# Kernel tuning notes

Measured on AMD Instinct MI355X. Metric: run time of the kernel, lower is better.

The kernel has to match this reference:

```python
import jax, jax.numpy as jnp
import numpy as np

B, M, N, E = 64, 100, 6400, 102400   # graphs, nodes/graph, total nodes, edges
H, D, EMB, IMG, NC = 4, 512, 768, 1024, 2
HD = H * D
EPS = 1e-5


def _bn2(x, g, b, m, v):
    # BatchNorm1d eval mode on [B, C]
    return (x - m) / jnp.sqrt(v + EPS) * g + b


def _bn3(x, g, b, m, v):
    # BatchNorm1d eval mode on [B, C, L] -> channel dim is axis 1 (node index)
    return (x - m[None, :, None]) / jnp.sqrt(v + EPS)[None, :, None] * g[None, :, None] + b[None, :, None]


def _gat(feat, src, dst, W, al, ar, bias):
    # DGL GATConv (eval: feat_drop is identity). feat: [N, F_in]
    h = (feat @ W.T).reshape(-1, H, D)                 # [N, H, D]
    el = (h * al[None]).sum(-1)                         # [N, H]
    er = (h * ar[None]).sum(-1)                         # [N, H]
    e = jax.nn.leaky_relu(el[src] + er[dst], negative_slope=0.2)  # [E, H]
    mx = jax.ops.segment_max(e, dst, num_segments=N)
    a = jnp.exp(e - mx[dst])
    s = jax.ops.segment_sum(a, dst, num_segments=N)
    alpha = a / s[dst]                                  # edge softmax over incoming edges
    out = jax.ops.segment_sum(h[src] * alpha[:, :, None], dst, num_segments=N)  # [N, H, D]
    return out + bias.reshape(1, H, D)


def setup_inputs() -> dict:
    key = jax.random.key(0)
    ks = iter(jax.random.split(key, 80))
    n = lambda *s: jax.random.normal(next(ks), s, dtype=jnp.float32)

    def bn(c):
        return (1.0 + 0.1 * n(c), 0.1 * n(c), 0.1 * n(c),
                0.5 + jax.random.uniform(next(ks), (c,), dtype=jnp.float32))

    s = 0.02
    inp = {}
    inp['img_embedding'] = n(B, IMG)
    inp['func_text_embedding'] = n(B, EMB)
    inp['unix_emb'] = n(N, EMB)
    inp['pos_emb'] = jax.random.uniform(next(ks), (N, 4), dtype=jnp.float32)
    inp['src'] = jax.random.randint(next(ks), (E,), 0, N)
    inp['dst'] = jax.random.randint(next(ks), (E,), 0, N)
    inp['gat1_W'] = n(HD, EMB) * s; inp['gat1_al'] = n(H, D) * 0.1; inp['gat1_ar'] = n(H, D) * 0.1; inp['gat1_b'] = jnp.zeros(HD)
    inp['gat2_W'] = n(HD, HD) * s; inp['gat2_al'] = n(H, D) * 0.1; inp['gat2_ar'] = n(H, D) * 0.1; inp['gat2_b'] = jnp.zeros(HD)
    inp['fc_W'] = n(D, HD) * s; inp['fc_b'] = jnp.zeros(D)
    inp['hidden_W'] = n(8, D, D) * s; inp['hidden_b'] = jnp.zeros((8, D))
    inp['bn_text_g'], inp['bn_text_b'], inp['bn_text_m'], inp['bn_text_v'] = bn(EMB)
    inp['fc_text_W'] = n(D, EMB) * s; inp['fc_text_b'] = jnp.zeros(D)
    inp['swin_g'], inp['swin_b'], inp['swin_m'], inp['swin_v'] = bn(IMG)
    inp['swinfc_W'] = n(D, IMG) * s; inp['swinfc_b'] = jnp.zeros(D)
    inp['bngat_g'], inp['bngat_b'], inp['bngat_m'], inp['bngat_v'] = bn(M)
    inp['fc_gat_W'] = n(480, D) * s; inp['fc_gat_b'] = jnp.zeros(480)
    inp['bnbb_g'], inp['bnbb_b'], inp['bnbb_m'], inp['bnbb_v'] = bn(M)
    inp['fc_bbox_W'] = n(32, 4) * s; inp['fc_bbox_b'] = jnp.zeros(32)
    inp['fbn_g'], inp['fbn_b'], inp['fbn_m'], inp['fbn_v'] = bn(3 * D)
    inp['final_W'] = n(NC, 3 * D) * s; inp['final_b'] = jnp.zeros(NC)
    return inp


def reference(img_embedding, func_text_embedding, unix_emb, pos_emb, src, dst,
              gat1_W, gat1_al, gat1_ar, gat1_b, gat2_W, gat2_al, gat2_ar, gat2_b,
              fc_W, fc_b, hidden_W, hidden_b,
              bn_text_g, bn_text_b, bn_text_m, bn_text_v, fc_text_W, fc_text_b,
              swin_g, swin_b, swin_m, swin_v, swinfc_W, swinfc_b,
              bngat_g, bngat_b, bngat_m, bngat_v, fc_gat_W, fc_gat_b,
              bnbb_g, bnbb_b, bnbb_m, bnbb_v, fc_bbox_W, fc_bbox_b,
              fbn_g, fbn_b, fbn_m, fbn_v, final_W, final_b):
    # image branch
    x = jax.nn.elu(_bn2(img_embedding, swin_g, swin_b, swin_m, swin_v) @ swinfc_W.T + swinfc_b)
    # text branch
    ft = jax.nn.elu(_bn2(func_text_embedding, bn_text_g, bn_text_b, bn_text_m, bn_text_v) @ fc_text_W.T + fc_text_b)
    # graph branch: two stacked GATConv layers (dropout is identity in eval)
    h = _gat(unix_emb, src, dst, gat1_W, gat1_al, gat1_ar, gat1_b).reshape(N, HD)
    h = _gat(h, src, dst, gat2_W, gat2_al, gat2_ar, gat2_b).reshape(N, HD)
    h = jax.nn.elu(h @ fc_W.T + fc_b)
    for i in range(8):
        h = jax.nn.elu(h @ hidden_W[i].T + hidden_b[i])
    # unbatch + pad to max_node=100 -> pure reshape (all graphs have exactly M nodes)
    h_i = h.reshape(B, M, D)
    pos_i = pos_emb.reshape(B, M, 4)
    h_i = jax.nn.elu(_bn3(h_i, bngat_g, bngat_b, bngat_m, bngat_v) @ fc_gat_W.T + fc_gat_b)      # [B, M, 480]
    pos_i = jax.nn.elu(_bn3(pos_i, bnbb_g, bnbb_b, bnbb_m, bnbb_v) @ fc_bbox_W.T + fc_bbox_b)    # [B, M, 32]
    h_feature = jnp.concatenate([h_i, pos_i], axis=2).mean(axis=1)                                # [B, 512]
    all_feats = jnp.concatenate([x, h_feature, ft], axis=1)                                       # [B, 1536]
    return _bn2(all_feats, fbn_g, fbn_b, fbn_m, fbn_v) @ final_W.T + final_b
```

## Files before the change

kernel.cpp:

```cpp
#include <hip/hip_runtime.h>
#include <math.h>

#define Bg   64
#define Mg   100
#define Ng   6400
#define Eg   102400
#define Hh   4
#define Dd   512
#define HDd  2048
#define EMBd 768
#define IMGd 1024
#define EPSc 1e-5f

typedef __bf16 bf16x8 __attribute__((ext_vector_type(8)));
typedef float  f32x4  __attribute__((ext_vector_type(4)));

__device__ __forceinline__ float eluf(float x) { return x > 0.f ? x : expm1f(x); }

__device__ __forceinline__ unsigned short f2bf(float x) {
    unsigned int u = __builtin_bit_cast(unsigned int, x);
    u += 0x7FFFu + ((u >> 16) & 1u);
    return (unsigned short)(u >> 16);
}
__device__ __forceinline__ float bf2f(unsigned short s) {
    return __builtin_bit_cast(float, ((unsigned int)s) << 16);
}

__device__ __forceinline__ void gld16(const void* g, void* l) {
    __builtin_amdgcn_global_load_lds(
        (const __attribute__((address_space(1))) void*)g,
        (__attribute__((address_space(3))) void*)l, 16, 0, 0);
}

__global__ __launch_bounds__(256)
void gemm_bf16(const unsigned short* __restrict__ A,
               const unsigned short* __restrict__ W,
               const float* __restrict__ bias, void* __restrict__ C,
               int M, int N, int K, int act, int outbf)
{
    __shared__ __align__(16) unsigned short As[128 * 32];
    __shared__ __align__(16) unsigned short Bs[128 * 32];
    const int tid  = threadIdx.x;
    const int lane = tid & 63, wid = tid >> 6;
    const int bm = blockIdx.y * 128, bn = blockIdx.x * 128;
    const int wm = (wid >> 1) * 64, wn = (wid & 1) * 64;
    const int lrow = lane >> 2;
    const int lcol = (lane & 3) << 3;

    f32x4 acc[4][4] = {};

    const int ra = wid * 32;
    const unsigned short* gA0 = A + (size_t)(bm + ra + lrow) * K + lcol;
    const unsigned short* gA1 = A + (size_t)(bm + ra + 16 + lrow) * K + lcol;
    int rb0 = bn + ra + lrow;       if (rb0 >= N) rb0 = N - 1;
    int rb1 = bn + ra + 16 + lrow;  if (rb1 >= N) rb1 = N - 1;
    const unsigned short* gB0 = W + (size_t)rb0 * K + lcol;
    const unsigned short* gB1 = W + (size_t)rb1 * K + lcol;
    unsigned short* lA0 = &As[(ra)      * 32];
    unsigned short* lA1 = &As[(ra + 16) * 32];
    unsigned short* lB0 = &Bs[(ra)      * 32];
    unsigned short* lB1 = &Bs[(ra + 16) * 32];

    const int frow = lane & 15;
    const int quad = (lane >> 4) << 3;

    for (int k0 = 0; k0 < K; k0 += 32) {
        gld16(gA0 + k0, lA0);
        gld16(gA1 + k0, lA1);
        gld16(gB0 + k0, lB0);
        gld16(gB1 + k0, lB1);
        __syncthreads();
        bf16x8 af[4], bfr[4];
#pragma unroll
        for (int i = 0; i < 4; ++i)
            af[i]  = *(const bf16x8*)&As[(wm + i * 16 + frow) * 32 + quad];
#pragma unroll
        for (int i = 0; i < 4; ++i)
            bfr[i] = *(const bf16x8*)&Bs[(wn + i * 16 + frow) * 32 + quad];
#pragma unroll
        for (int mi = 0; mi < 4; ++mi)
#pragma unroll
            for (int ni = 0; ni < 4; ++ni)
                acc[mi][ni] = __builtin_amdgcn_mfma_f32_16x16x32_bf16(
                    af[mi], bfr[ni], acc[mi][ni], 0, 0, 0);
        __syncthreads();
    }

    const int crow0 = bm + wm + ((lane >> 4) << 2);
    const int ccol0 = bn + wn + (lane & 15);
#pragma unroll
    for (int mi = 0; mi < 4; ++mi) {
#pragma unroll
        for (int ni = 0; ni < 4; ++ni) {
            int col = ccol0 + ni * 16;
            if (col >= N) continue;
            float bv = bias ? bias[col] : 0.f;
#pragma unroll
            for (int r = 0; r < 4; ++r) {
                int row = crow0 + mi * 16 + r;
                float v = acc[mi][ni][r] + bv;
                if (act) v = eluf(v);
                if (outbf) ((unsigned short*)C)[(size_t)row * N + col] = f2bf(v);
                else       ((float*)C)[(size_t)row * N + col] = v;
            }
        }
    }
}

__global__ __launch_bounds__(256)
void gemm_bf16_t64(const unsigned short* __restrict__ A,
                   const unsigned short* __restrict__ W,
                   const float* __restrict__ bias, void* __restrict__ C,
                   int M, int N, int K, int act, int outbf)
{
    __shared__ __align__(16) unsigned short As[64 * 32];
    __shared__ __align__(16) unsigned short Bs[64 * 32];
    const int tid  = threadIdx.x;
    const int lane = tid & 63, wid = tid >> 6;
    const int bm = blockIdx.y * 64, bn = blockIdx.x * 64;
    const int wm = (wid >> 1) * 32, wn = (wid & 1) * 32;
    const int lrow = lane >> 2;
    const int lcol = (lane & 3) << 3;

    f32x4 acc[2][2] = {};

    const int ra = wid * 16;
    const unsigned short* gA = A + (size_t)(bm + ra + lrow) * K + lcol;
    int rb = bn + ra + lrow; if (rb >= N) rb = N - 1;
    const unsigned short* gB = W + (size_t)rb * K + lcol;
    unsigned short* lA = &As[ra * 32];
    unsigned short* lB = &Bs[ra * 32];

    const int frow = lane & 15;
    const int quad = (lane >> 4) << 3;

    for (int k0 = 0; k0 < K; k0 += 32) {
        gld16(gA + k0, lA);
        gld16(gB + k0, lB);
        __syncthreads();
        bf16x8 af0 = *(const bf16x8*)&As[(wm + frow) * 32 + quad];
        bf16x8 af1 = *(const bf16x8*)&As[(wm + 16 + frow) * 32 + quad];
        bf16x8 bf0 = *(const bf16x8*)&Bs[(wn + frow) * 32 + quad];
        bf16x8 bf1 = *(const bf16x8*)&Bs[(wn + 16 + frow) * 32 + quad];
        acc[0][0] = __builtin_amdgcn_mfma_f32_16x16x32_bf16(af0, bf0, acc[0][0], 0, 0, 0);
        acc[0][1] = __builtin_amdgcn_mfma_f32_16x16x32_bf16(af0, bf1, acc[0][1], 0, 0, 0);
        acc[1][0] = __builtin_amdgcn_mfma_f32_16x16x32_bf16(af1, bf0, acc[1][0], 0, 0, 0);
        acc[1][1] = __builtin_amdgcn_mfma_f32_16x16x32_bf16(af1, bf1, acc[1][1], 0, 0, 0);
        __syncthreads();
    }

    const int crow0 = bm + wm + ((lane >> 4) << 2);
    const int ccol0 = bn + wn + (lane & 15);
#pragma unroll
    for (int mi = 0; mi < 2; ++mi) {
#pragma unroll
        for (int ni = 0; ni < 2; ++ni) {
            int col = ccol0 + ni * 16;
            if (col >= N) continue;
            float bv = bias ? bias[col] : 0.f;
#pragma unroll
            for (int r = 0; r < 4; ++r) {
                int row = crow0 + mi * 16 + r;
                float v = acc[mi][ni][r] + bv;
                if (act) v = eluf(v);
                if (outbf) ((unsigned short*)C)[(size_t)row * N + col] = f2bf(v);
                else       ((float*)C)[(size_t)row * N + col] = v;
            }
        }
    }
}

__global__ __launch_bounds__(256)
void gemm_t64_fcgat(const unsigned short* __restrict__ A,
                    const unsigned short* __restrict__ W,
                    const float* __restrict__ bfg, const float* __restrict__ wsum,
                    const float* __restrict__ bng, const float* __restrict__ bnb,
                    const float* __restrict__ bnm, const float* __restrict__ bnv,
                    float* __restrict__ Eout, int M, int N, int K)
{
    __shared__ __align__(16) unsigned short As[64 * 32];
    __shared__ __align__(16) unsigned short Bs[64 * 32];
    const int tid  = threadIdx.x;
    const int lane = tid & 63, wid = tid >> 6;
    const int bm = blockIdx.y * 64, bn = blockIdx.x * 64;
    const int wm = (wid >> 1) * 32, wn = (wid & 1) * 32;
    const int lrow = lane >> 2;
    const int lcol = (lane & 3) << 3;

    f32x4 acc[2][2] = {};

    const int ra = wid * 16;
    const unsigned short* gA = A + (size_t)(bm + ra + lrow) * K + lcol;
    int rb = bn + ra + lrow; if (rb >= N) rb = N - 1;
    const unsigned short* gB = W + (size_t)rb * K + lcol;
    unsigned short* lA = &As[ra * 32];
    unsigned short* lB = &Bs[ra * 32];

    const int frow = lane & 15;
    const int quad = (lane >> 4) << 3;

    for (int k0 = 0; k0 < K; k0 += 32) {
        gld16(gA + k0, lA);
        gld16(gB + k0, lB);
        __syncthreads();
        bf16x8 af0 = *(const bf16x8*)&As[(wm + frow) * 32 + quad];
        bf16x8 af1 = *(const bf16x8*)&As[(wm + 16 + frow) * 32 + quad];
        bf16x8 bf0 = *(const bf16x8*)&Bs[(wn + frow) * 32 + quad];
        bf16x8 bf1 = *(const bf16x8*)&Bs[(wn + 16 + frow) * 32 + quad];
        acc[0][0] = __builtin_amdgcn_mfma_f32_16x16x32_bf16(af0, bf0, acc[0][0], 0, 0, 0);
        acc[0][1] = __builtin_amdgcn_mfma_f32_16x16x32_bf16(af0, bf1, acc[0][1], 0, 0, 0);
        acc[1][0] = __builtin_amdgcn_mfma_f32_16x16x32_bf16(af1, bf0, acc[1][0], 0, 0, 0);
        acc[1][1] = __builtin_amdgcn_mfma_f32_16x16x32_bf16(af1, bf1, acc[1][1], 0, 0, 0);
        __syncthreads();
    }

    const int crow0 = bm + wm + ((lane >> 4) << 2);
    const int ccol0 = bn + wn + (lane & 15);
#pragma unroll
    for (int mi = 0; mi < 2; ++mi) {
#pragma unroll
        for (int r = 0; r < 4; ++r) {
            int row = crow0 + mi * 16 + r;
            int p = row % Mg;
            float sc = rsqrtf(bnv[p] + EPSc) * bng[p];
            float sh = bnb[p] - bnm[p] * sc;
#pragma unroll
            for (int ni = 0; ni < 2; ++ni) {
                int col = ccol0 + ni * 16;
                if (col < N) {
                    float v = sc * acc[mi][ni][r] + sh * wsum[col] + bfg[col];
                    Eout[(size_t)row * N + col] = eluf(v);
                }
            }
        }
    }
}

__global__ __launch_bounds__(256)
void wsum_kernel(const float* __restrict__ W, float* __restrict__ s)
{
    int row = (blockIdx.x << 2) + (threadIdx.x >> 6);
    int lane = threadIdx.x & 63;
    if (row >= 480) return;
    const float* p = W + (size_t)row * Dd;
    float a = 0.f;
    for (int k = lane; k < Dd; k += 64) a += p[k];
#pragma unroll
    for (int o = 32; o > 0; o >>= 1) a += __shfl_down(a, o, 64);
    if (lane == 0) s[row] = a;
}

__global__ __launch_bounds__(256)
void gemm_nt(const float* __restrict__ A, const float* __restrict__ W,
             const float* __restrict__ bias, float* __restrict__ C,
             int M, int N, int K, int act)
{
    __shared__ float As[16 * 68];
    __shared__ float Ws[16 * 68];
    const int tid = threadIdx.x;
    const int tx = tid & 15, ty = tid >> 4;
    const int bm = blockIdx.y * 64, bn = blockIdx.x * 64;
    const int lrow = tid >> 2;
    const int lk4  = (tid & 3) << 2;
    const int arow = bm + lrow;
    const int wrow = bn + lrow;
    const float* Aptr = A + (size_t)arow * K + lk4;
    const float* Wptr = W + (size_t)wrow * K + lk4;
    float acc[4][4] = {{0.f,0.f,0.f,0.f},{0.f,0.f,0.f,0.f},{0.f,0.f,0.f,0.f},{0.f,0.f,0.f,0.f}};

    for (int k0 = 0; k0 < K; k0 += 16) {
        float4 av = make_float4(0.f,0.f,0.f,0.f);
        float4 wv = make_float4(0.f,0.f,0.f,0.f);
        if (arow < M) av = *(const float4*)(Aptr + k0);
        if (wrow < N) wv = *(const float4*)(Wptr + k0);
        As[(lk4+0)*68 + lrow] = av.x;
        As[(lk4+1)*68 + lrow] = av.y;
        As[(lk4+2)*68 + lrow] = av.z;
        As[(lk4+3)*68 + lrow] = av.w;
        Ws[(lk4+0)*68 + lrow] = wv.x;
        Ws[(lk4+1)*68 + lrow] = wv.y;
        Ws[(lk4+2)*68 + lrow] = wv.z;
        Ws[(lk4+3)*68 + lrow] = wv.w;
        __syncthreads();
#pragma unroll
        for (int kk = 0; kk < 16; ++kk) {
            float4 a = *(const float4*)&As[kk*68 + (ty<<2)];
            float4 w = *(const float4*)&Ws[kk*68 + (tx<<2)];
            acc[0][0] += a.x*w.x; acc[0][1] += a.x*w.y; acc[0][2] += a.x*w.z; acc[0][3] += a.x*w.w;
            acc[1][0] += a.y*w.x; acc[1][1] += a.y*w.y; acc[1][2] += a.y*w.z; acc[1][3] += a.y*w.w;
            acc[2][0] += a.z*w.x; acc[2][1] += a.z*w.y; acc[2][2] += a.z*w.z; acc[2][3] += a.z*w.w;
            acc[3][0] += a.w*w.x; acc[3][1] += a.w*w.y; acc[3][2] += a.w*w.z; acc[3][3] += a.w*w.w;
        }
        __syncthreads();
    }

#pragma unroll
    for (int i = 0; i < 4; ++i) {
        int row = bm + (ty<<2) + i;
        int col = bn + (tx<<2);
        if (row < M && col < N) {
            float4 v;
            v.x = acc[i][0]; v.y = acc[i][1]; v.z = acc[i][2]; v.w = acc[i][3];
            if (bias) { v.x += bias[col]; v.y += bias[col+1]; v.z += bias[col+2]; v.w += bias[col+3]; }
            if (act == 1) { v.x = eluf(v.x); v.y = eluf(v.y); v.z = eluf(v.z); v.w = eluf(v.w); }
            *(float4*)(C + (size_t)row * N + col) = v;
        }
    }
}

struct CvtPack {
    const float* s[6];
    unsigned short* d[6];
    int n4[6];
};

__global__ void cvt_all(CvtPack p, int total4)
{
    int i = blockIdx.x * 256 + threadIdx.x;
    if (i >= total4) return;
#pragma unroll
    for (int k = 0; k < 6; ++k) {
        if (i < p.n4[k]) {
            float4 v = ((const float4*)p.s[k])[i];
            ushort4 o;
            o.x = f2bf(v.x); o.y = f2bf(v.y); o.z = f2bf(v.z); o.w = f2bf(v.w);
            ((ushort4*)p.d[k])[i] = o;
            return;
        }
        i -= p.n4[k];
    }
}

__global__ void bn_col(const float* __restrict__ x, const float* __restrict__ g,
                       const float* __restrict__ b, const float* __restrict__ m,
                       const float* __restrict__ v, float* __restrict__ y,
                       int rows, int cols)
{
    int i = blockIdx.x * 256 + threadIdx.x;
    if (i >= rows * cols) return;
    int c = i % cols;
    float inv = rsqrtf(v[c] + EPSc);
    y[i] = (x[i] - m[c]) * inv * g[c] + b[c];
}

__global__ void zero_i32(int* __restrict__ p, int n)
{
    int i = blockIdx.x * 256 + threadIdx.x;
    if (i < n) p[i] = 0;
}

__global__ void count_dst(const int* __restrict__ dst, int* __restrict__ counts, int E)
{
    int i = blockIdx.x * 256 + threadIdx.x;
    if (i < E) atomicAdd(&counts[dst[i]], 1);
}

__global__ __launch_bounds__(1024)
void scan_excl(const int* __restrict__ counts, int* __restrict__ offs,
               int* __restrict__ cursor, int n)
{
    const int T = 7;
    int tid = threadIdx.x;
    int base = tid * T;
    int v[T];
    int tot = 0;
#pragma unroll
    for (int j = 0; j < T; ++j) {
        int i = base + j;
        v[j] = (i < n) ? counts[i] : 0;
        tot += v[j];
    }
    int lane = tid & 63, w = tid >> 6;
    int incl = tot;
#pragma unroll
    for (int o = 1; o < 64; o <<= 1) {
        int t = __shfl_up(incl, o, 64);
        if (lane >= o) incl += t;
    }
    __shared__ int wtot[16];
    __shared__ int wbase[16];
    if (lane == 63) wtot[w] = incl;
    __syncthreads();
    if (tid == 0) {
        int s = 0;
        for (int i = 0; i < 16; ++i) { wbase[i] = s; s += wtot[i]; }
    }
    __syncthreads();
    int ex = wbase[w] + incl - tot;
#pragma unroll
    for (int j = 0; j < T; ++j) {
        int i = base + j;
        if (i < n) { offs[i] = ex; cursor[i] = ex; }
        ex += v[j];
    }
    if (tid == 1023) offs[n] = ex;
}

__global__ void scatter_edges(const int* __restrict__ dst, int* __restrict__ cursor,
                              int* __restrict__ eid, int E)
{
    int i = blockIdx.x * 256 + threadIdx.x;
    if (i < E) {
        int p = atomicAdd(&cursor[dst[i]], 1);
        eid[p] = i;
    }
}

__global__ __launch_bounds__(256)
void elr_kernel(const unsigned short* __restrict__ Hm, const float* __restrict__ al,
                const float* __restrict__ ar, float* __restrict__ el,
                float* __restrict__ er)
{
    int wid = threadIdx.x >> 6, lane = threadIdx.x & 63;
    int g = (blockIdx.x << 2) + wid;
    int n = g >> 2, h = g & 3;
    const unsigned short* hp = Hm + ((size_t)n << 11) + (h << 9) + (lane << 3);
    const float* alp = al + (h << 9) + (lane << 3);
    const float* arp = ar + (h << 9) + (lane << 3);
    ushort4 x0 = *(const ushort4*)hp;
    ushort4 x1 = *(const ushort4*)(hp + 4);
    float4 l0 = *(const float4*)alp, l1 = *(const float4*)(alp + 4);
    float4 r0 = *(const float4*)arp, r1 = *(const float4*)(arp + 4);
    float a0 = bf2f(x0.x), a1 = bf2f(x0.y), a2 = bf2f(x0.z), a3 = bf2f(x0.w);
    float a4 = bf2f(x1.x), a5 = bf2f(x1.y), a6 = bf2f(x1.z), a7 = bf2f(x1.w);
    float se = a0*l0.x + a1*l0.y + a2*l0.z + a3*l0.w + a4*l1.x + a5*l1.y + a6*l1.z + a7*l1.w;
    float sr = a0*r0.x + a1*r0.y + a2*r0.z + a3*r0.w + a4*r1.x + a5*r1.y + a6*r1.z + a7*r1.w;
#pragma unroll
    for (int o = 32; o > 0; o >>= 1) {
        se += __shfl_down(se, o, 64);
        sr += __shfl_down(sr, o, 64);
    }
    if (lane == 0) { el[g] = se; er[g] = sr; }
}

__global__ __launch_bounds__(256)
void gat_agg(const unsigned short* __restrict__ Hm, const float* __restrict__ el,
             const float* __restrict__ er, const int* __restrict__ src,
             const int* __restrict__ offs, const int* __restrict__ eid,
             const float* __restrict__ bias, unsigned short* __restrict__ out)
{
    int n = blockIdx.x;
    int tid = threadIdx.x;
    int beg = offs[n], end = offs[n + 1];
    int deg = end - beg;
    const int b0 = tid << 2;
    const int b1 = 1024 + (tid << 2);
    const int h0 = tid >> 7;
    const int h1 = h0 + 2;

    if (deg == 0) {
#pragma unroll
        for (int j = 0; j < 4; ++j) {
            out[((size_t)n << 11) + b0 + j] = f2bf(bias[b0 + j]);
            out[((size_t)n << 11) + b1 + j] = f2bf(bias[b1 + j]);
        }
        return;
    }

    __shared__ float m_sh[4], s_sh[4], al_sh[4];
    __shared__ int   src_sh[128];
    __shared__ float logit_sh[512];
    __shared__ float w_sh[512];

    if (tid < 4) { m_sh[tid] = -INFINITY; s_sh[tid] = 0.f; }
    float acc[8] = {0.f,0.f,0.f,0.f,0.f,0.f,0.f,0.f};
    __syncthreads();

    for (int c0 = 0; c0 < deg; c0 += 128) {
        int cnt = min(128, deg - c0);
        for (int i = tid; i < cnt; i += 256) src_sh[i] = src[eid[beg + c0 + i]];
        __syncthreads();
        for (int idx = tid; idx < (cnt << 2); idx += 256) {
            int i = idx >> 2, h = idx & 3;
            float x = el[(src_sh[i] << 2) + h] + er[(n << 2) + h];
            logit_sh[idx] = x > 0.f ? x : 0.2f * x;
        }
        __syncthreads();
        if (tid < 4) {
            float cm = -INFINITY;
            for (int i = 0; i < cnt; ++i) cm = fmaxf(cm, logit_sh[(i << 2) + tid]);
            float mn = fmaxf(m_sh[tid], cm);
            al_sh[tid] = expf(m_sh[tid] - mn);
            m_sh[tid] = mn;
        }
        __syncthreads();
        for (int idx = tid; idx < (cnt << 2); idx += 256)
            w_sh[idx] = expf(logit_sh[idx] - m_sh[idx & 3]);
        __syncthreads();
        if (tid < 4) {
            float cs = 0.f;
            for (int i = 0; i < cnt; ++i) cs += w_sh[(i << 2) + tid];
            s_sh[tid] = s_sh[tid] * al_sh[tid] + cs;
        }
        float r0 = al_sh[h0], r1 = al_sh[h1];
        acc[0] *= r0; acc[1] *= r0; acc[2] *= r0; acc[3] *= r0;
        acc[4] *= r1; acc[5] *= r1; acc[6] *= r1; acc[7] *= r1;
        for (int i = 0; i < cnt; ++i) {
            const unsigned short* hp = Hm + ((size_t)src_sh[i] << 11);
            ushort4 a = *(const ushort4*)(hp + b0);
            ushort4 b = *(const ushort4*)(hp + b1);
            float w0 = w_sh[(i << 2) + h0], w1 = w_sh[(i << 2) + h1];
            acc[0] += w0 * bf2f(a.x); acc[1] += w0 * bf2f(a.y);
            acc[2] += w0 * bf2f(a.z); acc[3] += w0 * bf2f(a.w);
            acc[4] += w1 * bf2f(b.x); acc[5] += w1 * bf2f(b.y);
            acc[6] += w1 * bf2f(b.z); acc[7] += w1 * bf2f(b.w);
        }
        __syncthreads();
    }

    float is0 = 1.f / s_sh[h0], is1 = 1.f / s_sh[h1];
#pragma unroll
    for (int j = 0; j < 4; ++j) {
        out[((size_t)n << 11) + b0 + j] = f2bf(acc[j] * is0 + bias[b0 + j]);
        out[((size_t)n << 11) + b1 + j] = f2bf(acc[4 + j] * is1 + bias[b1 + j]);
    }
}

__global__ __launch_bounds__(256)
void mean_kernel(const float* __restrict__ hg, const float* __restrict__ pos,
                 const float* __restrict__ bg, const float* __restrict__ bb_,
                 const float* __restrict__ bm_, const float* __restrict__ bv_,
                 const float* __restrict__ W, const float* __restrict__ bias,
                 float* __restrict__ hf)
{
    int bb = blockIdx.x;
    int tid = threadIdx.x;
    int c0 = tid, c1 = tid + 256;
    const float* hb = hg + (size_t)bb * Mg * 480;
    float s0 = 0.f, s1 = 0.f;
    for (int m = 0; m < Mg; ++m) {
        s0 += hb[m * 480 + c0];
        if (c1 < 480) s1 += hb[m * 480 + c1];
    }
    if (c1 >= 480) {
        int o = c1 - 480;
        float w0 = W[(o << 2) + 0], w1 = W[(o << 2) + 1];
        float w2 = W[(o << 2) + 2], w3 = W[(o << 2) + 3];
        float bo = bias[o];
        const float* pp = pos + (size_t)bb * Mg * 4;
        s1 = 0.f;
        for (int m = 0; m < Mg; ++m) {
            float sc = rsqrtf(bv_[m] + EPSc) * bg[m];
            float sh = bb_[m] - bm_[m] * sc;
            float a = bo + (pp[m*4+0]*sc+sh)*w0 + (pp[m*4+1]*sc+sh)*w1
                         + (pp[m*4+2]*sc+sh)*w2 + (pp[m*4+3]*sc+sh)*w3;
            s1 += eluf(a);
        }
    }
    hf[bb * 512 + c0] = s0 * 0.01f;
    hf[bb * 512 + c1] = s1 * 0.01f;
}

__global__ __launch_bounds__(256)
void final_kernel(const float* __restrict__ x, const float* __restrict__ hf,
                  const float* __restrict__ ft, const float* __restrict__ g,
                  const float* __restrict__ b, const float* __restrict__ m,
                  const float* __restrict__ v, const float* __restrict__ W,
                  const float* __restrict__ bias, float* __restrict__ out)
{
    int bb = blockIdx.x;
    int tid = threadIdx.x;
    float a0 = 0.f, a1 = 0.f;
    for (int c = tid; c < 1536; c += 256) {
        float xv = (c < 512) ? x[bb * 512 + c]
                 : (c < 1024) ? hf[bb * 512 + (c - 512)]
                              : ft[bb * 512 + (c - 1024)];
        float z = (xv - m[c]) * rsqrtf(v[c] + EPSc) * g[c] + b[c];
        a0 += z * W[c];
        a1 += z * W[1536 + c];
    }
    __shared__ float r0[256], r1[256];
    r0[tid] = a0; r1[tid] = a1;
    __syncthreads();
    for (int o = 128; o > 0; o >>= 1) {
        if (tid < o) { r0[tid] += r0[tid + o]; r1[tid] += r1[tid + o]; }
        __syncthreads();
    }
    if (tid == 0) {
        out[bb * 2 + 0] = r0[0] + bias[0];
        out[bb * 2 + 1] = r1[0] + bias[1];
    }
}

extern "C" void kernel_launch(void* const* d_in, const int* in_sizes, int n_in,
                              void* d_out, int out_size, void* d_ws, size_t ws_size,
                              hipStream_t stream)
{
    (void)in_sizes; (void)n_in; (void)out_size; (void)ws_size;

    const float* img   = (const float*)d_in[0];
    const float* ftxt  = (const float*)d_in[1];
    const float* unixe = (const float*)d_in[2];
    const float* pos   = (const float*)d_in[3];
    const int*   src   = (const int*)  d_in[4];
    const int*   dst   = (const int*)  d_in[5];
    const float* g1W   = (const float*)d_in[6];
    const float* g1al  = (const float*)d_in[7];
    const float* g1ar  = (const float*)d_in[8];
    const float* g1b   = (const float*)d_in[9];
    const float* g2W   = (const float*)d_in[10];
    const float* g2al  = (const float*)d_in[11];
    const float* g2ar  = (const float*)d_in[12];
    const float* g2b   = (const float*)d_in[13];
    const float* fcW   = (const float*)d_in[14];
    const float* fcb   = (const float*)d_in[15];
    const float* hidW  = (const float*)d_in[16];
    const float* hidb  = (const float*)d_in[17];
    const float* btg   = (const float*)d_in[18];
    const float* btb   = (const float*)d_in[19];
    const float* btm   = (const float*)d_in[20];
    const float* btv   = (const float*)d_in[21];
    const float* ftW   = (const float*)d_in[22];
    const float* ftbi  = (const float*)d_in[23];
    const float* swg   = (const float*)d_in[24];
    const float* swb   = (const float*)d_in[25];
    const float* swm   = (const float*)d_in[26];
    const float* swv   = (const float*)d_in[27];
    const float* swW   = (const float*)d_in[28];
    const float* swbi  = (const float*)d_in[29];
    const float* bgg   = (const float*)d_in[30];
    const float* bgb   = (const float*)d_in[31];
    const float* bgm   = (const float*)d_in[32];
    const float* bgv   = (const float*)d_in[33];
    const float* fgW   = (const float*)d_in[34];
    const float* fgb   = (const float*)d_in[35];
    const float* bbgp  = (const float*)d_in[36];
    const float* bbbp  = (const float*)d_in[37];
    const float* bbmp  = (const float*)d_in[38];
    const float* bbvp  = (const float*)d_in[39];
    const float* fbW   = (const float*)d_in[40];
    const float* fbb   = (const float*)d_in[41];
    const float* fng   = (const float*)d_in[42];
    const float* fnb   = (const float*)d_in[43];
    const float* fnm   = (const float*)d_in[44];
    const float* fnv   = (const float*)d_in[45];
    const float* fiW   = (const float*)d_in[46];
    const float* fib   = (const float*)d_in[47];
    float* out = (float*)d_out;

    char* p = (char*)d_ws;
    unsigned short* fA  = (unsigned short*)p; p += (size_t)Ng * HDd * 2;
    unsigned short* fB  = (unsigned short*)p; p += (size_t)Ng * HDd * 2;
    unsigned short* fC  = (unsigned short*)p; p += (size_t)Ng * Dd * 2;
    unsigned short* fD  = (unsigned short*)p; p += (size_t)Ng * Dd * 2;
    float*          fE  = (float*)p;          p += (size_t)Ng * 480 * 4;
    float*          el  = (float*)p;          p += (size_t)Ng * Hh * 4;
    float*          er  = (float*)p;          p += (size_t)Ng * Hh * 4;
    float*          xb  = (float*)p;          p += (size_t)Bg * Dd * 4;
    float*          ftb = (float*)p;          p += (size_t)Bg * Dd * 4;
    float*          hf  = (float*)p;          p += (size_t)Bg * Dd * 4;
    float*          ti  = (float*)p;          p += (size_t)Bg * IMGd * 4;
    float*          tt  = (float*)p;          p += (size_t)Bg * EMBd * 4;
    float*          wsm = (float*)p;          p += (size_t)480 * 4;
    unsigned short* ubf = (unsigned short*)p; p += (size_t)Ng * EMBd * 2;
    unsigned short* wg1 = (unsigned short*)p; p += (size_t)HDd * EMBd * 2;
    unsigned short* wg2 = (unsigned short*)p; p += (size_t)HDd * HDd * 2;
    unsigned short* wfc = (unsigned short*)p; p += (size_t)Dd * HDd * 2;
    unsigned short* whid= (unsigned short*)p; p += (size_t)8 * Dd * Dd * 2;
    unsigned short* wfg = (unsigned short*)p; p += (size_t)480 * Dd * 2;
    int* counts = (int*)p; p += (size_t)Ng * 4;
    int* offs   = (int*)p; p += (size_t)(Ng + 1) * 4 + 12;
    int* cursor = (int*)p; p += (size_t)Ng * 4;
    int* eid    = (int*)p; p += (size_t)Eg * 4;

    CvtPack cp;
    cp.s[0] = unixe; cp.d[0] = ubf;  cp.n4[0] = Ng * EMBd / 4;
    cp.s[1] = g1W;   cp.d[1] = wg1;  cp.n4[1] = HDd * EMBd / 4;
    cp.s[2] = g2W;   cp.d[2] = wg2;  cp.n4[2] = HDd * HDd / 4;
    cp.s[3] = fcW;   cp.d[3] = wfc;  cp.n4[3] = Dd * HDd / 4;
    cp.s[4] = hidW;  cp.d[4] = whid; cp.n4[4] = 8 * Dd * Dd / 4;
    cp.s[5] = fgW;   cp.d[5] = wfg;  cp.n4[5] = 480 * Dd / 4;
    int total4 = cp.n4[0] + cp.n4[1] + cp.n4[2] + cp.n4[3] + cp.n4[4] + cp.n4[5];
    cvt_all<<<(total4 + 255)/256, 256, 0, stream>>>(cp, total4);
    wsum_kernel<<<120, 256, 0, stream>>>(fgW, wsm);

    bn_col<<<(Bg*IMGd + 255)/256, 256, 0, stream>>>(img, swg, swb, swm, swv, ti, Bg, IMGd);
    gemm_nt<<<dim3(8, 1), 256, 0, stream>>>(ti, swW, swbi, xb, Bg, Dd, IMGd, 1);
    bn_col<<<(Bg*EMBd + 255)/256, 256, 0, stream>>>(ftxt, btg, btb, btm, btv, tt, Bg, EMBd);
    gemm_nt<<<dim3(8, 1), 256, 0, stream>>>(tt, ftW, ftbi, ftb, Bg, Dd, EMBd, 1);

    zero_i32<<<(Ng + 255)/256, 256, 0, stream>>>(counts, Ng);
    count_dst<<<(Eg + 255)/256, 256, 0, stream>>>(dst, counts, Eg);
    scan_excl<<<1, 1024, 0, stream>>>(counts, offs, cursor, Ng);
    scatter_edges<<<(Eg + 255)/256, 256, 0, stream>>>(dst, cursor, eid, Eg);

    gemm_bf16<<<dim3(HDd/128, Ng/128), 256, 0, stream>>>(ubf, wg1, nullptr, fA, Ng, HDd, EMBd, 0, 1);
    elr_kernel<<<Ng, 256, 0, stream>>>(fA, g1al, g1ar, el, er);
    gat_agg<<<Ng, 256, 0, stream>>>(fA, el, er, src, offs, eid, g1b, fB);

    gemm_bf16<<<dim3(HDd/128, Ng/128), 256, 0, stream>>>(fB, wg2, nullptr, fA, Ng, HDd, HDd, 0, 1);
    elr_kernel<<<Ng, 256, 0, stream>>>(fA, g2al, g2ar, el, er);
    gat_agg<<<Ng, 256, 0, stream>>>(fA, el, er, src, offs, eid, g2b, fB);

    gemm_bf16_t64<<<dim3(Dd/64, Ng/64), 256, 0, stream>>>(fB, wfc, fcb, fC, Ng, Dd, HDd, 1, 1);

    unsigned short* cur = fC; unsigned short* nxt = fD;
    for (int i = 0; i < 8; ++i) {
        gemm_bf16_t64<<<dim3(Dd/64, Ng/64), 256, 0, stream>>>(
            cur, whid + (size_t)i * Dd * Dd, hidb + (size_t)i * Dd, nxt, Ng, Dd, Dd, 1, 1);
        unsigned short* t = cur; cur = nxt; nxt = t;
    }

    gemm_t64_fcgat<<<dim3(8, Ng/64), 256, 0, stream>>>(
        cur, wfg, fgb, wsm, bgg, bgb, bgm, bgv, fE, Ng, 480, Dd);

    mean_kernel<<<Bg, 256, 0, stream>>>(fE, pos, bbgp, bbbp, bbmp, bbvp, fbW, fbb, hf);

    final_kernel<<<Bg, 256, 0, stream>>>(xb, hf, ftb, fng, fnb, fnm, fnv, fiW, fib, out);
}
```

Measured before the change: 868.5 us.

## Deepen K-step in 64-tile GEMMs, vectorize GAT aggregation, store fc_gat output as bf16

The 64x64 GEMM kernels now load two 32-wide K slices per iteration, which halves the number of barrier pairs per K sweep. The GAT aggregation kernel is remapped so each thread owns 8 contiguous features of one head and reads them with one 16-byte vector load, where before it used two 8-byte loads across two heads. The fc_gat output buffer moves from fp32 to bf16, which halves that write and the read in mean_kernel. The cost is slightly lower precision on that intermediate, plus doubled LDS per block.

Result: no change. 856.3 us (-1.4%).

```diff
diff --git a/kernel.cpp b/kernel.cpp
--- a/kernel.cpp
+++ b/kernel.cpp
@@ -14,6 +14,7 @@
 
 typedef __bf16 bf16x8 __attribute__((ext_vector_type(8)));
 typedef float  f32x4  __attribute__((ext_vector_type(4)));
+typedef unsigned short us8v __attribute__((ext_vector_type(8)));
 
 __device__ __forceinline__ float eluf(float x) { return x > 0.f ? x : expm1f(x); }
 
@@ -108,13 +109,13 @@
 }
 
 __global__ __launch_bounds__(256)
-void gemm_bf16_t64(const unsigned short* __restrict__ A,
-                   const unsigned short* __restrict__ W,
-                   const float* __restrict__ bias, void* __restrict__ C,
-                   int M, int N, int K, int act, int outbf)
-{
-    __shared__ __align__(16) unsigned short As[64 * 32];
-    __shared__ __align__(16) unsigned short Bs[64 * 32];
+void gemm_t64b(const unsigned short* __restrict__ A,
+               const unsigned short* __restrict__ W,
+               const float* __restrict__ bias, void* __restrict__ C,
+               int M, int N, int K, int act, int outbf)
+{
+    __shared__ __align__(16) unsigned short As[2 * 64 * 32];
+    __shared__ __align__(16) unsigned short Bs[2 * 64 * 32];
     const int tid  = threadIdx.x;
     const int lane = tid & 63, wid = tid >> 6;
     const int bm = blockIdx.y * 64, bn = blockIdx.x * 64;
@@ -124,28 +125,35 @@
 
     f32x4 acc[2][2] = {};
 
-    const int ra = wid * 16;
-    const unsigned short* gA = A + (size_t)(bm + ra + lrow) * K + lcol;
-    int rb = bn + ra + lrow; if (rb >= N) rb = N - 1;
+    const int r0 = wid * 16;
+    const unsigned short* gA = A + (size_t)(bm + r0 + lrow) * K + lcol;
+    int rb = bn + r0 + lrow; if (rb >= N) rb = N - 1;
     const unsigned short* gB = W + (size_t)rb * K + lcol;
-    unsigned short* lA = &As[ra * 32];
-    unsigned short* lB = &Bs[ra * 32];
+    unsigned short* lA0 = &As[r0 * 32];
+    unsigned short* lA1 = &As[2048 + r0 * 32];
+    unsigned short* lB0 = &Bs[r0 * 32];
+    unsigned short* lB1 = &Bs[2048 + r0 * 32];
 
     const int frow = lane & 15;
     const int quad = (lane >> 4) << 3;
 
-    for (int k0 = 0; k0 < K; k0 += 32) {
-        gld16(gA + k0, lA);
-        gld16(gB + k0, lB);
-        __syncthreads();
-        bf16x8 af0 = *(const bf16x8*)&As[(wm + frow) * 32 + quad];
-        bf16x8 af1 = *(const bf16x8*)&As[(wm + 16 + frow) * 32 + quad];
-        bf16x8 bf0 = *(const bf16x8*)&Bs[(wn + frow) * 32 + quad];
-        bf16x8 bf1 = *(const bf16x8*)&Bs[(wn + 16 + frow) * 32 + quad];
-        acc[0][0] = __builtin_amdgcn_mfma_f32_16x16x32_bf16(af0, bf0, acc[0][0], 0, 0, 0);
-        acc[0][1] = __builtin_amdgcn_mfma_f32_16x16x32_bf16(af0, bf1, acc[0][1], 0, 0, 0);
-        acc[1][0] = __builtin_amdgcn_mfma_f32_16x16x32_bf16(af1, bf0, acc[1][0], 0, 0, 0);
-        acc[1][1] = __builtin_amdgcn_mfma_f32_16x16x32_bf16(af1, bf1, acc[1][1], 0, 0, 0);
+    for (int k0 = 0; k0 < K; k0 += 64) {
+        gld16(gA + k0,      lA0);
+        gld16(gA + k0 + 32, lA1);
+        gld16(gB + k0,      lB0);
+        gld16(gB + k0 + 32, lB1);
+        __syncthreads();
+#pragma unroll
+        for (int ks = 0; ks < 2; ++ks) {
+            bf16x8 af0 = *(const bf16x8*)&As[ks * 2048 + (wm + frow) * 32 + quad];
+            bf16x8 af1 = *(const bf16x8*)&As[ks * 2048 + (wm + 16 + frow) * 32 + quad];
+            bf16x8 bf0 = *(const bf16x8*)&Bs[ks * 2048 + (wn + frow) * 32 + quad];
+            bf16x8 bf1 = *(const bf16x8*)&Bs[ks * 2048 + (wn + 16 + frow) * 32 + quad];
+            acc[0][0] = __builtin_amdgcn_mfma_f32_16x16x32_bf16(af0, bf0, acc[0][0], 0, 0, 0);
+            acc[0][1] = __builtin_amdgcn_mfma_f32_16x16x32_bf16(af0, bf1, acc[0][1], 0, 0, 0);
+            acc[1][0] = __builtin_amdgcn_mfma_f32_16x16x32_bf16(af1, bf0, acc[1][0], 0, 0, 0);
+            acc[1][1] = __builtin_amdgcn_mfma_f32_16x16x32_bf16(af1, bf1, acc[1][1], 0, 0, 0);
+        }
         __syncthreads();
     }
 
@@ -171,15 +179,15 @@
 }
 
 __global__ __launch_bounds__(256)
-void gemm_t64_fcgat(const unsigned short* __restrict__ A,
-                    const unsigned short* __restrict__ W,
-                    const float* __restrict__ bfg, const float* __restrict__ wsum,
-                    const float* __restrict__ bng, const float* __restrict__ bnb,
-                    const float* __restrict__ bnm, const float* __restrict__ bnv,
-                    float* __restrict__ Eout, int M, int N, int K)
-{
-    __shared__ __align__(16) unsigned short As[64 * 32];
-    __shared__ __align__(16) unsigned short Bs[64 * 32];
+void gemm_t64b_fcgat(const unsigned short* __restrict__ A,
+                     const unsigned short* __restrict__ W,
+                     const float* __restrict__ bfg, const float* __restrict__ wsum,
+                     const float* __restrict__ bng, const float* __restrict__ bnb,
+                     const float* __restrict__ bnm, const float* __restrict__ bnv,
+                     unsigned short* __restrict__ Eout, int M, int N, int K)
+{
+    __shared__ __align__(16) unsigned short As[2 * 64 * 32];
+    __shared__ __align__(16) unsigned short Bs[2 * 64 * 32];
     const int tid  = threadIdx.x;
     const int lane = tid & 63, wid = tid >> 6;
     const int bm = blockIdx.y * 64, bn = blockIdx.x * 64;
@@ -189,28 +197,35 @@
 
     f32x4 acc[2][2] = {};
 
-    const int ra = wid * 16;
-    const unsigned short* gA = A + (size_t)(bm + ra + lrow) * K + lcol;
-    int rb = bn + ra + lrow; if (rb >= N) rb = N - 1;
+    const int r0 = wid * 16;
+    const unsigned short* gA = A + (size_t)(bm + r0 + lrow) * K + lcol;
+    int rb = bn + r0 + lrow; if (rb >= N) rb = N - 1;
     const unsigned short* gB = W + (size_t)rb * K + lcol;
-    unsigned short* lA = &As[ra * 32];
-    unsigned short* lB = &Bs[ra * 32];
+    unsigned short* lA0 = &As[r0 * 32];
+    unsigned short* lA1 = &As[2048 + r0 * 32];
+    unsigned short* lB0 = &Bs[r0 * 32];
+    unsigned short* lB1 = &Bs[2048 + r0 * 32];
 
     const int frow = lane & 15;
     const int quad = (lane >> 4) << 3;
 
-    for (int k0 = 0; k0 < K; k0 += 32) {
-        gld16(gA + k0, lA);
-        gld16(gB + k0, lB);
-        __syncthreads();
-        bf16x8 af0 = *(const bf16x8*)&As[(wm + frow) * 32 + quad];
-        bf16x8 af1 = *(const bf16x8*)&As[(wm + 16 + frow) * 32 + quad];
-        bf16x8 bf0 = *(const bf16x8*)&Bs[(wn + frow) * 32 + quad];
-        bf16x8 bf1 = *(const bf16x8*)&Bs[(wn + 16 + frow) * 32 + quad];
-        acc[0][0] = __builtin_amdgcn_mfma_f32_16x16x32_bf16(af0, bf0, acc[0][0], 0, 0, 0);
-        acc[0][1] = __builtin_amdgcn_mfma_f32_16x16x32_bf16(af0, bf1, acc[0][1], 0, 0, 0);
-        acc[1][0] = __builtin_amdgcn_mfma_f32_16x16x32_bf16(af1, bf0, acc[1][0], 0, 0, 0);
-        acc[1][1] = __builtin_amdgcn_mfma_f32_16x16x32_bf16(af1, bf1, acc[1][1], 0, 0, 0);
+    for (int k0 = 0; k0 < K; k0 += 64) {
+        gld16(gA + k0,      lA0);
+        gld16(gA + k0 + 32, lA1);
+        gld16(gB + k0,      lB0);
+        gld16(gB + k0 + 32, lB1);
+        __syncthreads();
+#pragma unroll
+        for (int ks = 0; ks < 2; ++ks) {
+            bf16x8 af0 = *(const bf16x8*)&As[ks * 2048 + (wm + frow) * 32 + quad];
+            bf16x8 af1 = *(const bf16x8*)&As[ks * 2048 + (wm + 16 + frow) * 32 + quad];
+            bf16x8 bf0 = *(const bf16x8*)&Bs[ks * 2048 + (wn + frow) * 32 + quad];
+            bf16x8 bf1 = *(const bf16x8*)&Bs[ks * 2048 + (wn + 16 + frow) * 32 + quad];
+            acc[0][0] = __builtin_amdgcn_mfma_f32_16x16x32_bf16(af0, bf0, acc[0][0], 0, 0, 0);
+            acc[0][1] = __builtin_amdgcn_mfma_f32_16x16x32_bf16(af0, bf1, acc[0][1], 0, 0, 0);
+            acc[1][0] = __builtin_amdgcn_mfma_f32_16x16x32_bf16(af1, bf0, acc[1][0], 0, 0, 0);
+            acc[1][1] = __builtin_amdgcn_mfma_f32_16x16x32_bf16(af1, bf1, acc[1][1], 0, 0, 0);
+        }
         __syncthreads();
     }
 
@@ -229,7 +244,7 @@
                 int col = ccol0 + ni * 16;
                 if (col < N) {
                     float v = sc * acc[mi][ni][r] + sh * wsum[col] + bfg[col];
-                    Eout[(size_t)row * N + col] = eluf(v);
+                    Eout[(size_t)row * N + col] = f2bf(eluf(v));
                 }
             }
         }
@@ -443,17 +458,13 @@
     int tid = threadIdx.x;
     int beg = offs[n], end = offs[n + 1];
     int deg = end - beg;
-    const int b0 = tid << 2;
-    const int b1 = 1024 + (tid << 2);
-    const int h0 = tid >> 7;
-    const int h1 = h0 + 2;
+    const int d0 = tid << 3;
+    const int h  = tid >> 6;
 
     if (deg == 0) {
 #pragma unroll
-        for (int j = 0; j < 4; ++j) {
-            out[((size_t)n << 11) + b0 + j] = f2bf(bias[b0 + j]);
-            out[((size_t)n << 11) + b1 + j] = f2bf(bias[b1 + j]);
-        }
+        for (int j = 0; j < 8; ++j)
+            out[((size_t)n << 11) + d0 + j] = f2bf(bias[d0 + j]);
         return;
     }
 
@@ -471,8 +482,8 @@
         for (int i = tid; i < cnt; i += 256) src_sh[i] = src[eid[beg + c0 + i]];
         __syncthreads();
         for (int idx = tid; idx < (cnt << 2); idx += 256) {
-            int i = idx >> 2, h = idx & 3;
-            float x = el[(src_sh[i] << 2) + h] + er[(n << 2) + h];
+            int i = idx >> 2, hh = idx & 3;
+            float x = el[(src_sh[i] << 2) + hh] + er[(n << 2) + hh];
             logit_sh[idx] = x > 0.f ? x : 0.2f * x;
         }
         __syncthreads();
@@ -492,32 +503,27 @@
             for (int i = 0; i < cnt; ++i) cs += w_sh[(i << 2) + tid];
             s_sh[tid] = s_sh[tid] * al_sh[tid] + cs;
         }
-        float r0 = al_sh[h0], r1 = al_sh[h1];
-        acc[0] *= r0; acc[1] *= r0; acc[2] *= r0; acc[3] *= r0;
-        acc[4] *= r1; acc[5] *= r1; acc[6] *= r1; acc[7] *= r1;
+        float rsc = al_sh[h];
+#pragma unroll
+        for (int j = 0; j < 8; ++j) acc[j] *= rsc;
         for (int i = 0; i < cnt; ++i) {
-            const unsigned short* hp = Hm + ((size_t)src_sh[i] << 11);
-            ushort4 a = *(const ushort4*)(hp + b0);
-            ushort4 b = *(const ushort4*)(hp + b1);
-            float w0 = w_sh[(i << 2) + h0], w1 = w_sh[(i << 2) + h1];
-            acc[0] += w0 * bf2f(a.x); acc[1] += w0 * bf2f(a.y);
-            acc[2] += w0 * bf2f(a.z); acc[3] += w0 * bf2f(a.w);
-            acc[4] += w1 * bf2f(b.x); acc[5] += w1 * bf2f(b.y);
-            acc[6] += w1 * bf2f(b.z); acc[7] += w1 * bf2f(b.w);
-        }
-        __syncthreads();
-    }
-
-    float is0 = 1.f / s_sh[h0], is1 = 1.f / s_sh[h1];
-#pragma unroll
-    for (int j = 0; j < 4; ++j) {
-        out[((size_t)n << 11) + b0 + j] = f2bf(acc[j] * is0 + bias[b0 + j]);
-        out[((size_t)n << 11) + b1 + j] = f2bf(acc[4 + j] * is1 + bias[b1 + j]);
-    }
-}
-
-__global__ __launch_bounds__(256)
-void mean_kernel(const float* __restrict__ hg, const float* __restrict__ pos,
+            const unsigned short* hp = Hm + ((size_t)src_sh[i] << 11) + d0;
+            us8v a = *(const us8v*)hp;
+            float w0 = w_sh[(i << 2) + h];
+#pragma unroll
+            for (int j = 0; j < 8; ++j) acc[j] += w0 * bf2f(a[j]);
+        }
+        __syncthreads();
+    }
+
+    float is = 1.f / s_sh[h];
+#pragma unroll
+    for (int j = 0; j < 8; ++j)
+        out[((size_t)n << 11) + d0 + j] = f2bf(acc[j] * is + bias[d0 + j]);
+}
+
+__global__ __launch_bounds__(256)
+void mean_kernel(const unsigned short* __restrict__ hg, const float* __restrict__ pos,
                  const float* __restrict__ bg, const float* __restrict__ bb_,
                  const float* __restrict__ bm_, const float* __restrict__ bv_,
                  const float* __restrict__ W, const float* __restrict__ bias,
@@ -526,11 +532,11 @@
     int bb = blockIdx.x;
     int tid = threadIdx.x;
     int c0 = tid, c1 = tid + 256;
-    const float* hb = hg + (size_t)bb * Mg * 480;
+    const unsigned short* hb = hg + (size_t)bb * Mg * 480;
     float s0 = 0.f, s1 = 0.f;
     for (int m = 0; m < Mg; ++m) {
-        s0 += hb[m * 480 + c0];
-        if (c1 < 480) s1 += hb[m * 480 + c1];
+        s0 += bf2f(hb[m * 480 + c0]);
+        if (c1 < 480) s1 += bf2f(hb[m * 480 + c1]);
     }
     if (c1 >= 480) {
         int o = c1 - 480;
@@ -643,7 +649,7 @@
     unsigned short* fB  = (unsigned short*)p; p += (size_t)Ng * HDd * 2;
     unsigned short* fC  = (unsigned short*)p; p += (size_t)Ng * Dd * 2;
     unsigned short* fD  = (unsigned short*)p; p += (size_t)Ng * Dd * 2;
-    float*          fE  = (float*)p;          p += (size_t)Ng * 480 * 4;
+    unsigned short* fE  = (unsigned short*)p; p += (size_t)Ng * 480 * 2;
     float*          el  = (float*)p;          p += (size_t)Ng * Hh * 4;
     float*          er  = (float*)p;          p += (size_t)Ng * Hh * 4;
     float*          xb  = (float*)p;          p += (size_t)Bg * Dd * 4;
@@ -692,16 +698,16 @@
     elr_kernel<<<Ng, 256, 0, stream>>>(fA, g2al, g2ar, el, er);
     gat_agg<<<Ng, 256, 0, stream>>>(fA, el, er, src, offs, eid, g2b, fB);
 
-    gemm_bf16_t64<<<dim3(Dd/64, Ng/64), 256, 0, stream>>>(fB, wfc, fcb, fC, Ng, Dd, HDd, 1, 1);
+    gemm_t64b<<<dim3(Dd/64, Ng/64), 256, 0, stream>>>(fB, wfc, fcb, fC, Ng, Dd, HDd, 1, 1);
 
     unsigned short* cur = fC; unsigned short* nxt = fD;
     for (int i = 0; i < 8; ++i) {
-        gemm_bf16_t64<<<dim3(Dd/64, Ng/64), 256, 0, stream>>>(
+        gemm_t64b<<<dim3(Dd/64, Ng/64), 256, 0, stream>>>(
             cur, whid + (size_t)i * Dd * Dd, hidb + (size_t)i * Dd, nxt, Ng, Dd, Dd, 1, 1);
         unsigned short* t = cur; cur = nxt; nxt = t;
     }
 
-    gemm_t64_fcgat<<<dim3(8, Ng/64), 256, 0, stream>>>(
+    gemm_t64b_fcgat<<<dim3(8, Ng/64), 256, 0, stream>>>(
         cur, wfg, fgb, wsm, bgg, bgb, bgm, bgv, fE, Ng, 480, Dd);
 
     mean_kernel<<<Bg, 256, 0, stream>>>(fE, pos, bbgp, bbbp, bbmp, bbvp, fbW, fbb, hf);
```
